# Optimization experiments

Measured on AMD Instinct MI355X. Metric: run time of the kernel, lower is better.

## Reference

```python
import jax, jax.numpy as jnp
import numpy as np
from jax import lax

B, C, D, H, W = 4, 384, 16, 16, 16
DSTATE, DCONV, EXPAND = 16, 4, 2
DIN = C * EXPAND            # 768
DTRANK = (C + 15) // 16     # 24
EPS = 1e-5


def setup_inputs() -> dict:
    ks = jax.random.split(jax.random.key(0), 12)
    g = lambda k, shape, s=0.02: jax.random.normal(k, shape, jnp.float32) * s
    return {
        "x": jax.random.normal(ks[0], (B, C, D, H, W), jnp.float32),
        "gsc_w1": g(ks[1], (C, C, 3, 3, 3)), "gsc_b1": jnp.zeros((C,), jnp.float32),
        "gsc_w2": g(ks[2], (C, C, 3, 3, 3)), "gsc_b2": jnp.zeros((C,), jnp.float32),
        "gsc_w3": g(ks[3], (C, C, 1, 1, 1)), "gsc_b3": jnp.zeros((C,), jnp.float32),
        "gsc_w4": g(ks[4], (C, C, 1, 1, 1)), "gsc_b4": jnp.zeros((C,), jnp.float32),
        "ln_g": jnp.ones((C,), jnp.float32), "ln_b": jnp.zeros((C,), jnp.float32),
        "in_proj_w": g(ks[5], (2 * DIN, C)),
        "conv1d_w": g(ks[6], (DIN, 1, DCONV), 0.1), "conv1d_b": jnp.zeros((DIN,), jnp.float32),
        "x_proj_w": g(ks[7], (DTRANK + 2 * DSTATE, DIN)),
        "dt_proj_w": g(ks[8], (DIN, DTRANK), 0.1), "dt_proj_b": jnp.full((DIN,), -4.0, jnp.float32),
        "A_log": jnp.log(jnp.tile(jnp.arange(1, DSTATE + 1, dtype=jnp.float32), (DIN, 1))),
        "D_skip": jnp.ones((DIN,), jnp.float32),
        "out_proj_w": g(ks[9], (C, DIN)),
    }


def _conv3d(x, w, b, pad):
    y = lax.conv_general_dilated(x, w, (1, 1, 1), [(pad, pad)] * 3,
                                 dimension_numbers=("NCDHW", "OIDHW", "NCDHW"))
    return y + b[None, :, None, None, None]


def _inorm(x):  # InstanceNorm3d, affine=False, biased variance
    m = x.mean((2, 3, 4), keepdims=True)
    v = x.var((2, 3, 4), keepdims=True)
    return (x - m) * lax.rsqrt(v + EPS)


def _forward(x, gsc_w1, gsc_b1, gsc_w2, gsc_b2, gsc_w3, gsc_b3, gsc_w4, gsc_b4,
             ln_g, ln_b, in_proj_w, conv1d_w, conv1d_b, x_proj_w,
             dt_proj_w, dt_proj_b, A_log, D_skip, out_proj_w):
    relu = jax.nn.relu
    # ---- GSC block (residual gated spatial conv) ----
    x1 = relu(_inorm(_conv3d(x, gsc_w1, gsc_b1, 1)))
    x1 = relu(_inorm(_conv3d(x1, gsc_w2, gsc_b2, 1)))
    x2 = relu(_inorm(_conv3d(x, gsc_w3, gsc_b3, 0)))
    xg = relu(_inorm(_conv3d(x1 + x2, gsc_w4, gsc_b4, 0))) + x
    # ---- MambaLayer: flatten voxels to tokens ----
    Bn = xg.shape[0]
    L = D * H * W
    t = xg.reshape(Bn, C, L).swapaxes(1, 2)                     # [B, L, C]
    mu = t.mean(-1, keepdims=True)
    var = t.var(-1, keepdims=True)
    tn = (t - mu) * lax.rsqrt(var + EPS) * ln_g + ln_b          # LayerNorm
    # ---- Mamba block ----
    xz = tn @ in_proj_w.T                                       # [B, L, 2*DIN]
    xin, z = jnp.split(xz, 2, axis=-1)
    xc = xin.swapaxes(1, 2)                                     # [B, DIN, L]
    xc = lax.conv_general_dilated(xc, conv1d_w, (1,), [(DCONV - 1, 0)],
                                  dimension_numbers=("NCH", "OIH", "NCH"),
                                  feature_group_count=DIN)      # causal depthwise conv
    u = jax.nn.silu(xc + conv1d_b[None, :, None]).swapaxes(1, 2)  # [B, L, DIN]
    dbl = u @ x_proj_w.T                                        # [B, L, DTRANK+2N]
    dt, Bm, Cm = jnp.split(dbl, [DTRANK, DTRANK + DSTATE], axis=-1)
    dt = jax.nn.softplus(dt @ dt_proj_w.T + dt_proj_b)          # [B, L, DIN]
    A = -jnp.exp(A_log)                                         # [DIN, N]

    def step(h, inp):  # h: [B, DIN, N]
        dt_t, B_t, C_t, u_t = inp
        dA = jnp.exp(dt_t[:, :, None] * A)
        h = dA * h + (dt_t * u_t)[:, :, None] * B_t[:, None, :]
        return h, jnp.einsum("bdn,bn->bd", h, C_t)

    h0 = jnp.zeros((Bn, DIN, DSTATE), x.dtype)
    _, ys = lax.scan(step, h0, (dt.swapaxes(0, 1), Bm.swapaxes(0, 1),
                                Cm.swapaxes(0, 1), u.swapaxes(0, 1)))
    y = ys.swapaxes(0, 1) + u * D_skip                          # [B, L, DIN]
    y = y * jax.nn.silu(z)
    out = y @ out_proj_w.T                                      # [B, L, C]
    return out.swapaxes(1, 2).reshape(Bn, C, D, H, W)


def reference(x, gsc_w1, gsc_b1, gsc_w2, gsc_b2, gsc_w3, gsc_b3, gsc_w4, gsc_b4,
              ln_g, ln_b, in_proj_w, conv1d_w, conv1d_b, x_proj_w,
              dt_proj_w, dt_proj_b, A_log, D_skip, out_proj_w):
    return _forward(x, gsc_w1, gsc_b1, gsc_w2, gsc_b2, gsc_w3, gsc_b3, gsc_w4, gsc_b4,
                    ln_g, ln_b, in_proj_w, conv1d_w, conv1d_b, x_proj_w,
                    dt_proj_w, dt_proj_b, A_log, D_skip, out_proj_w)
```

## Files before the change

### kernel.cpp

```cpp
#include <hip/hip_runtime.h>
#include <math.h>

#define CDIM 384
#define SDIM 4096
#define BDIM 4
#define DINC 768
#define NST  16
#define NCHUNK 64
#define LCHUNK 64
#define PSTRIDE 6291456

typedef unsigned short ushort_t;
typedef unsigned int uint_t;
typedef __attribute__((ext_vector_type(4))) float f32x4;
typedef __attribute__((ext_vector_type(8))) short bf16x8;

__device__ __forceinline__ ushort_t f2bf(float f) {
    union { float f; uint_t u; } v; v.f = f;
    uint_t r = v.u + 0x7FFFu + ((v.u >> 16) & 1u);
    return (ushort_t)(r >> 16);
}
__device__ __forceinline__ float bf2f(ushort_t u) {
    union { uint_t i; float f; } v; v.i = ((uint_t)u) << 16; return v.f;
}
__device__ __forceinline__ uint_t pk2(float a, float b) {
    return (uint_t)f2bf(a) | ((uint_t)f2bf(b) << 16);
}
__device__ __forceinline__ void gl16(const ushort_t* g, ushort_t* l) {
    __builtin_amdgcn_global_load_lds(
        (const __attribute__((address_space(1))) void*)(g),
        (__attribute__((address_space(3))) void*)(l), 16, 0, 0);
}

__device__ __forceinline__ void wconv_body(const float* __restrict__ W,
                                           ushort_t* __restrict__ Wb, int idx) {
    const float* wp = W + (size_t)idx * 27;
#pragma unroll
    for (int tap = 0; tap < 27; ++tap)
        Wb[(size_t)tap * (CDIM * CDIM) + idx] = f2bf(wp[tap]);
}
__device__ __forceinline__ void cvt_body(const float* __restrict__ src,
                                         ushort_t* __restrict__ dst, int i) {
    float4 v = ((const float4*)src)[i];
    uint2 o; o.x = pk2(v.x, v.y); o.y = pk2(v.z, v.w);
    ((uint2*)dst)[i] = o;
}
__global__ __launch_bounds__(256)
void prep_weights_kernel(const float* w1, const float* w2, const float* w3,
                         const float* w4, const float* ipw, const float* opw,
                         const float* xpw,
                         ushort_t* Wb1, ushort_t* Wb2, ushort_t* w3b, ushort_t* w4b,
                         ushort_t* ipwb, ushort_t* opwb, ushort_t* xpwb) {
    const int bid = blockIdx.x, t = threadIdx.x;
    if      (bid < 576)  wconv_body(w1, Wb1, bid * 256 + t);
    else if (bid < 1152) wconv_body(w2, Wb2, (bid - 576) * 256 + t);
    else if (bid < 1296) cvt_body(w3, w3b, (bid - 1152) * 256 + t);
    else if (bid < 1440) cvt_body(w4, w4b, (bid - 1296) * 256 + t);
    else if (bid < 2016) cvt_body(ipw, ipwb, (bid - 1440) * 256 + t);
    else if (bid < 2304) cvt_body(opw, opwb, (bid - 2016) * 256 + t);
    else                 cvt_body(xpw, xpwb, (bid - 2304) * 256 + t);
}

__global__ __launch_bounds__(384)
void pad_kernel(const float* __restrict__ src, ushort_t* __restrict__ Xp) {
    const int blk = blockIdx.x;
    const int b = blk >> 8, d = (blk >> 4) & 15, h = blk & 15;
    const int ci = threadIdx.x;
    const float* sp = src + (size_t)(b * CDIM + ci) * SDIM + d * 256 + h * 16;
    ushort_t* dp = Xp + ((((size_t)(b * 18 + d + 1) * 18) + (h + 1)) * 18 + 1) * CDIM + ci;
#pragma unroll
    for (int w = 0; w < 16; ++w)
        dp[(size_t)w * CDIM] = f2bf(sp[w]);
}

__global__ __launch_bounds__(384)
void pad_fuse2_kernel(const ushort_t* __restrict__ P0, const ushort_t* __restrict__ P1,
                      const float* __restrict__ stats, ushort_t* __restrict__ Xp) {
    const int blk = blockIdx.x;
    const int b = blk >> 8, d = (blk >> 4) & 15, h = blk & 15;
    const int ci = threadIdx.x;
    const size_t o = (size_t)(b * CDIM + ci) * SDIM + d * 256 + h * 16;
    const float m = stats[(b * CDIM + ci) * 2], r = stats[(b * CDIM + ci) * 2 + 1];
    union { uint4 q[2]; ushort_t u[16]; } a, c;
    a.q[0] = ((const uint4*)(P0 + o))[0]; a.q[1] = ((const uint4*)(P0 + o))[1];
    c.q[0] = ((const uint4*)(P1 + o))[0]; c.q[1] = ((const uint4*)(P1 + o))[1];
    ushort_t* dp = Xp + ((((size_t)(b * 18 + d + 1) * 18) + (h + 1)) * 18 + 1) * CDIM + ci;
#pragma unroll
    for (int w = 0; w < 16; ++w) {
        const float v = bf2f(a.u[w]) + bf2f(c.u[w]);
        dp[(size_t)w * CDIM] = f2bf(fmaxf((v - m) * r, 0.f));
    }
}

__global__ __launch_bounds__(384)
void pad_fuse3_kernel(const ushort_t* __restrict__ P0, const ushort_t* __restrict__ P1,
                      const float* __restrict__ st2, const ushort_t* __restrict__ C3,
                      const float* __restrict__ st3, ushort_t* __restrict__ Xp) {
    const int blk = blockIdx.x;
    const int b = blk >> 8, d = (blk >> 4) & 15, h = blk & 15;
    const int ci = threadIdx.x;
    const size_t o = (size_t)(b * CDIM + ci) * SDIM + d * 256 + h * 16;
    const float m2 = st2[(b * CDIM + ci) * 2], r2 = st2[(b * CDIM + ci) * 2 + 1];
    const float m3 = st3[(b * CDIM + ci) * 2], r3 = st3[(b * CDIM + ci) * 2 + 1];
    union { uint4 q[2]; ushort_t u[16]; } a, c, e;
    a.q[0] = ((const uint4*)(P0 + o))[0]; a.q[1] = ((const uint4*)(P0 + o))[1];
    c.q[0] = ((const uint4*)(P1 + o))[0]; c.q[1] = ((const uint4*)(P1 + o))[1];
    e.q[0] = ((const uint4*)(C3 + o))[0]; e.q[1] = ((const uint4*)(C3 + o))[1];
    ushort_t* dp = Xp + ((((size_t)(b * 18 + d + 1) * 18) + (h + 1)) * 18 + 1) * CDIM + ci;
#pragma unroll
    for (int w = 0; w < 16; ++w) {
        const float x1 = fmaxf((bf2f(a.u[w]) + bf2f(c.u[w]) - m2) * r2, 0.f);
        const float x2 = fmaxf((bf2f(e.u[w]) - m3) * r3, 0.f);
        dp[(size_t)w * CDIM] = f2bf(x1 + x2);
    }
}

template<int MODE>
__global__ __launch_bounds__(256)
void conv_kernel(const ushort_t* __restrict__ Xp, const ushort_t* __restrict__ Wb,
                 const ushort_t* __restrict__ W3, ushort_t* __restrict__ Y01,
                 ushort_t* __restrict__ Y2) {
    const int wid = blockIdx.x;
    const int ntid = wid & 127;
    const int rest = wid >> 7;
    const int co0 = (rest % 3) * 128;
    const int zz  = rest / 3;
    const int b  = ntid >> 5;
    const int d  = (ntid >> 1) & 15;
    const int h0 = (ntid & 1) * 8;
    const int t = threadIdx.x;
    const int lane = t & 63;
    const int wv = t >> 6;
    const int wy = wv >> 1, wx = wv & 1;

    const bool is1x1 = (MODE == 2) || (MODE == 1 && zz == 2);
    const ushort_t* Wsrc; int tap0, iters, kd0, kh0, kw0; ushort_t* Y;
    if (is1x1) {
        Wsrc = W3; tap0 = 0; iters = 12; kd0 = 1; kh0 = 1; kw0 = 1; Y = Y2;
    } else {
        Wsrc = Wb; tap0 = zz ? 14 : 0; iters = (zz ? 13 : 14) * 12;
        kd0 = zz ? 1 : 0; kh0 = zz ? 1 : 0; kw0 = zz ? 2 : 0;
        Y = Y01 + (size_t)zz * PSTRIDE;
    }

    __shared__ __align__(16) ushort_t As[2][4096];
    __shared__ __align__(16) ushort_t Bs[2][4096];

    f32x4 acc[4][4];
#pragma unroll
    for (int i = 0; i < 4; ++i)
#pragma unroll
        for (int j = 0; j < 4; ++j) acc[i][j] = (f32x4){0.f, 0.f, 0.f, 0.f};

    const int l4 = lane >> 2;
    const int cg = (((lane & 3) ^ ((lane >> 3) & 3)) << 3);
    int aTC[2], bTC[2];
#pragma unroll
    for (int i = 0; i < 2; ++i) {
        const int r = wv * 32 + i * 16 + l4;
        aTC[i] = (co0 + r) * CDIM + cg;
        bTC[i] = ((r >> 4) * 18 + (r & 15)) * CDIM + cg;
    }

    int aoff = tap0 * (CDIM * CDIM);
    int goff = (((b * 18 + d + kd0) * 18 + (h0 + kh0)) * 18 + kw0) * CDIM;
    int c12 = 0, ckw = kw0, ckh = kh0;

    const int lm = lane & 15;
    const int sw8 = (((lane >> 4) ^ ((lm >> 1) & 3)) << 3);
    const int rA0 = (wy * 64 + lm) * 32 + sw8;
    const int rB0 = (wx * 64 + lm) * 32 + sw8;

    auto stage = [&](int bf) {
        ushort_t* la = &As[bf][wv * 1024];
        ushort_t* lb = &Bs[bf][wv * 1024];
        gl16(Wsrc + aoff + aTC[0], la);
        gl16(Wsrc + aoff + aTC[1], la + 512);
        gl16(Xp + goff + bTC[0], lb);
        gl16(Xp + goff + bTC[1], lb + 512);
        aoff += 32; goff += 32;
        if (++c12 == 12) {
            c12 = 0;
            aoff += CDIM * CDIM - CDIM;
            if (++ckw == 3) {
                ckw = 0;
                if (++ckh == 3) { ckh = 0; goff += 109440; }
                else goff += 5760;
            }
        }
    };

    stage(0);
    __syncthreads();

    int buf = 0;
    for (int idx = 0; idx < iters; ++idx) {
        if (idx + 1 < iters) stage(buf ^ 1);
        bf16x8 af[4], bfr[4];
#pragma unroll
        for (int mi = 0; mi < 4; ++mi)
            af[mi] = *reinterpret_cast<const bf16x8*>(&As[buf][rA0 + mi * 512]);
#pragma unroll
        for (int ni = 0; ni < 4; ++ni)
            bfr[ni] = *reinterpret_cast<const bf16x8*>(&Bs[buf][rB0 + ni * 512]);
#pragma unroll
        for (int mi = 0; mi < 4; ++mi)
#pragma unroll
            for (int ni = 0; ni < 4; ++ni)
                acc[mi][ni] = __builtin_amdgcn_mfma_f32_16x16x32_bf16(
                    af[mi], bfr[ni], acc[mi][ni], 0, 0, 0);
        __syncthreads();
        buf ^= 1;
    }

    const int coB = co0 + wy * 64 + (lane >> 4) * 4;
    const int nB  = wx * 64 + lm;
#pragma unroll
    for (int mi = 0; mi < 4; ++mi) {
#pragma unroll
        for (int ni = 0; ni < 4; ++ni) {
            const int nl = nB + ni * 16;
            const int s = d * 256 + (h0 + (nl >> 4)) * 16 + (nl & 15);
            ushort_t* yp = Y + ((size_t)b * CDIM + (coB + mi * 16)) * SDIM + s;
#pragma unroll
            for (int j = 0; j < 4; ++j)
                yp[(size_t)j * SDIM] = f2bf(acc[mi][ni][j]);
        }
    }
}

template<int EPI>
__global__ __launch_bounds__(256)
void gemm_gl_kernel(const ushort_t* __restrict__ A, const ushort_t* __restrict__ Bw,
                    void* __restrict__ Cv, void* __restrict__ C2v,
                    int M, int N, int K, int ldc, int nx) {
    const int wid = blockIdx.x;
    const int n0 = (wid % nx) * 128;
    const int m0 = (wid / nx) * 128;
    const int t = threadIdx.x;
    const int lane = t & 63;
    const int wv = t >> 6;
    const int wy = wv >> 1, wx = wv & 1;

    __shared__ __align__(16) ushort_t As[2][4096];
    __shared__ __align__(16) ushort_t Bs[2][4096];

    f32x4 acc[4][4];
#pragma unroll
    for (int i = 0; i < 4; ++i)
#pragma unroll
        for (int j = 0; j < 4; ++j) acc[i][j] = (f32x4){0.f, 0.f, 0.f, 0.f};

    const int l4 = lane >> 2;
    const int cg = (((lane & 3) ^ ((lane >> 3) & 3)) << 3);
    size_t aTC[2], bTC[2];
#pragma unroll
    for (int i = 0; i < 2; ++i) {
        const int r = wv * 32 + i * 16 + l4;
        aTC[i] = (size_t)(m0 + r) * K + cg;
        int br = n0 + r; if (br >= N) br = N - 1;
        bTC[i] = (size_t)br * K + cg;
    }

    const int lm = lane & 15;
    const int sw8 = (((lane >> 4) ^ ((lm >> 1) & 3)) << 3);
    const int rA0 = (wy * 64 + lm) * 32 + sw8;
    const int rB0 = (wx * 64 + lm) * 32 + sw8;

    auto stage = [&](int bf, int ko) {
        ushort_t* la = &As[bf][wv * 1024];
        ushort_t* lb = &Bs[bf][wv * 1024];
        gl16(A + aTC[0] + ko, la);
        gl16(A + aTC[1] + ko, la + 512);
        gl16(Bw + bTC[0] + ko, lb);
        gl16(Bw + bTC[1] + ko, lb + 512);
    };

    const int KI = K >> 5;
    stage(0, 0);
    __syncthreads();

    int buf = 0;
    for (int kk = 0; kk < KI; ++kk) {
        if (kk + 1 < KI) stage(buf ^ 1, (kk + 1) * 32);
        bf16x8 af[4], bfr[4];
#pragma unroll
        for (int mi = 0; mi < 4; ++mi)
            af[mi] = *reinterpret_cast<const bf16x8*>(&As[buf][rA0 + mi * 512]);
#pragma unroll
        for (int ni = 0; ni < 4; ++ni)
            bfr[ni] = *reinterpret_cast<const bf16x8*>(&Bs[buf][rB0 + ni * 512]);
#pragma unroll
        for (int mi = 0; mi < 4; ++mi)
#pragma unroll
            for (int ni = 0; ni < 4; ++ni)
                acc[mi][ni] = __builtin_amdgcn_mfma_f32_16x16x32_bf16(
                    af[mi], bfr[ni], acc[mi][ni], 0, 0, 0);
        __syncthreads();
        buf ^= 1;
    }

    const int mB = m0 + wy * 64 + (lane >> 4) * 4;
    const int nB = n0 + wx * 64 + lm;
#pragma unroll
    for (int mi = 0; mi < 4; ++mi) {
#pragma unroll
        for (int ni = 0; ni < 4; ++ni) {
            const int n = nB + ni * 16;
            if (EPI == 2) {
                const int mrow = mB + mi * 16;
                const int bb = mrow >> 12, l = mrow & 4095;
                float4 st = {acc[mi][ni][0], acc[mi][ni][1],
                             acc[mi][ni][2], acc[mi][ni][3]};
                *reinterpret_cast<float4*>(
                    (float*)Cv + ((size_t)(bb * CDIM + n)) * SDIM + l) = st;
            } else {
#pragma unroll
                for (int j = 0; j < 4; ++j) {
                    const int m = mB + mi * 16 + j;
                    const float v = acc[mi][ni][j];
                    if (EPI == 0) {
                        if (n < N) ((float*)Cv)[(size_t)m * ldc + n] = v;
                    } else {
                        if (n < DINC) ((ushort_t*)Cv)[(size_t)m * DINC + n] = f2bf(v);
                        else ((ushort_t*)C2v)[(size_t)m * DINC + (n - DINC)] = f2bf(v);
                    }
                }
            }
        }
    }
}

__device__ __forceinline__ void stats_reduce(float s, float ss, float* out) {
#pragma unroll
    for (int off = 32; off > 0; off >>= 1) {
        s += __shfl_down(s, off);
        ss += __shfl_down(ss, off);
    }
    __shared__ float rs[4], rss[4];
    const int wid = threadIdx.x >> 6;
    if ((threadIdx.x & 63) == 0) { rs[wid] = s; rss[wid] = ss; }
    __syncthreads();
    if (threadIdx.x == 0) {
        float S = rs[0] + rs[1] + rs[2] + rs[3];
        float SS = rss[0] + rss[1] + rss[2] + rss[3];
        float m = S * (1.f / SDIM);
        float var = SS * (1.f / SDIM) - m * m;
        out[0] = m;
        out[1] = rsqrtf(var + 1e-5f);
    }
}

__global__ __launch_bounds__(256)
void inorm_stats_combo_kernel(const ushort_t* __restrict__ P0,
                              const ushort_t* __restrict__ P1,
                              float* __restrict__ SA,
                              const ushort_t* __restrict__ X3,
                              float* __restrict__ SB) {
    const int bid = blockIdx.x;
    float s = 0.f, ss = 0.f;
    if (bid < 1536) {
        const ushort_t* p0 = P0 + (size_t)bid * SDIM;
        const ushort_t* p1 = P1 + (size_t)bid * SDIM;
        for (int i = threadIdx.x * 8; i < SDIM; i += 2048) {
            union { uint4 q; ushort_t u[8]; } a, c;
            a.q = *(const uint4*)(p0 + i);
            c.q = *(const uint4*)(p1 + i);
#pragma unroll
            for (int j = 0; j < 8; ++j) {
                const float v = bf2f(a.u[j]) + bf2f(c.u[j]);
                s += v; ss += v * v;
            }
        }
        stats_reduce(s, ss, SA + bid * 2);
    } else {
        const int bc = bid - 1536;
        const ushort_t* xp = X3 + (size_t)bc * SDIM;
        for (int i = threadIdx.x * 8; i < SDIM; i += 2048) {
            union { uint4 q; ushort_t u[8]; } a;
            a.q = *(const uint4*)(xp + i);
#pragma unroll
            for (int j = 0; j < 8; ++j) {
                const float v = bf2f(a.u[j]);
                s += v; ss += v * v;
            }
        }
        stats_reduce(s, ss, SB + bc * 2);
    }
}

__global__ __launch_bounds__(256)
void inorm_stats_kernel(const ushort_t* __restrict__ X, float* __restrict__ stats) {
    const int bc = blockIdx.x;
    const ushort_t* xp = X + (size_t)bc * SDIM;
    float s = 0.f, ss = 0.f;
    for (int i = threadIdx.x * 8; i < SDIM; i += 2048) {
        union { uint4 q; ushort_t u[8]; } a;
        a.q = *(const uint4*)(xp + i);
#pragma unroll
        for (int j = 0; j < 8; ++j) {
            const float v = bf2f(a.u[j]);
            s += v; ss += v * v;
        }
    }
    stats_reduce(s, ss, stats + bc * 2);
}

__global__ __launch_bounds__(256)
void layernorm_kernel(const ushort_t* __restrict__ C4, const float* __restrict__ stats,
                      const float* __restrict__ X, const float* __restrict__ gam,
                      const float* __restrict__ bet, ushort_t* __restrict__ Tn) {
    const int blk = blockIdx.x;
    const int b = blk >> 7;
    const int tile0 = (blk & 127) * 32;
    const int wv = threadIdx.x >> 6;
    const int lane = threadIdx.x & 63;
    const int l0 = tile0 + wv * 8;

    __shared__ ushort_t tile[32 * 384];

    float v[6][8];
    float s[8], ss[8];
#pragma unroll
    for (int t = 0; t < 8; ++t) { s[t] = 0.f; ss[t] = 0.f; }
    float g[6], be[6];

#pragma unroll
    for (int i = 0; i < 6; ++i) {
        const int c = lane + i * 64;
        g[i] = gam[c]; be[i] = bet[c];
        const size_t base = (size_t)(b * CDIM + c) * SDIM + l0;
        union { uint4 q; ushort_t u[8]; } cv;
        cv.q = *(const uint4*)(C4 + base);
        const float4 x0 = *(const float4*)(X + base);
        const float4 x1 = *(const float4*)(X + base + 4);
        const float xs[8] = {x0.x, x0.y, x0.z, x0.w, x1.x, x1.y, x1.z, x1.w};
        const float m = stats[(b * CDIM + c) * 2];
        const float r = stats[(b * CDIM + c) * 2 + 1];
#pragma unroll
        for (int t = 0; t < 8; ++t) {
            const float val = fmaxf((bf2f(cv.u[t]) - m) * r, 0.f) + xs[t];
            v[i][t] = val;
            s[t] += val; ss[t] += val * val;
        }
    }
#pragma unroll
    for (int off = 32; off > 0; off >>= 1) {
#pragma unroll
        for (int t = 0; t < 8; ++t) {
            s[t] += __shfl_xor(s[t], off);
            ss[t] += __shfl_xor(ss[t], off);
        }
    }
#pragma unroll
    for (int t = 0; t < 8; ++t) {
        const float mean = s[t] * (1.f / CDIM);
        const float rstd = rsqrtf(ss[t] * (1.f / CDIM) - mean * mean + 1e-5f);
        const int trow = (wv * 8 + t) * 384;
#pragma unroll
        for (int i = 0; i < 6; ++i) {
            const int c = lane + i * 64;
            tile[trow + c] = f2bf((v[i][t] - mean) * rstd * g[i] + be[i]);
        }
    }
    __syncthreads();
    uint4* dst = (uint4*)(Tn + ((size_t)b * 4096 + tile0) * CDIM);
    const uint4* srcp = (const uint4*)tile;
#pragma unroll
    for (int k = 0; k < 6; ++k)
        dst[k * 256 + threadIdx.x] = srcp[k * 256 + threadIdx.x];
}

__global__ __launch_bounds__(256)
void gemm_dtproj_kernel(const float* __restrict__ A, const float* __restrict__ B,
                        ushort_t* __restrict__ C, const float* __restrict__ bias,
                        int M, int N, int K, int lda, int ldb, int ldc) {
    __shared__ __align__(16) float As[16][132];
    __shared__ __align__(16) float Bs[16][68];
    const int t = threadIdx.x;
    const int m0 = blockIdx.y * 128;
    const int n0 = blockIdx.x * 64;

    float acc[8][4];
#pragma unroll
    for (int i = 0; i < 8; ++i)
#pragma unroll
        for (int j = 0; j < 4; ++j) acc[i][j] = 0.f;

    const int mr = (t & 15) * 8;
    const int nr = (t >> 4) * 4;

    for (int k0 = 0; k0 < K; k0 += 16) {
#pragma unroll
        for (int idx = 0; idx < 8; ++idx) {
            const int e = idx * 256 + t;
            const int k = e & 15, m = e >> 4;
            float v = 0.f;
            if (k0 + k < K) v = A[(size_t)(m0 + m) * lda + (k0 + k)];
            As[k][m] = v;
        }
#pragma unroll
        for (int idx = 0; idx < 4; ++idx) {
            const int e = idx * 256 + t;
            const int k = e & 15, n = e >> 4;
            float v = 0.f;
            if ((n0 + n) < N && (k0 + k) < K) v = B[(size_t)(n0 + n) * ldb + (k0 + k)];
            Bs[k][n] = v;
        }
        __syncthreads();
#pragma unroll
        for (int k = 0; k < 16; ++k) {
            float4 a0 = *(const float4*)&As[k][mr];
            float4 a1 = *(const float4*)&As[k][mr + 4];
            float4 b0 = *(const float4*)&Bs[k][nr];
            const float av[8] = {a0.x, a0.y, a0.z, a0.w, a1.x, a1.y, a1.z, a1.w};
            const float bv[4] = {b0.x, b0.y, b0.z, b0.w};
#pragma unroll
            for (int i = 0; i < 8; ++i)
#pragma unroll
                for (int j = 0; j < 4; ++j)
                    acc[i][j] = fmaf(av[i], bv[j], acc[i][j]);
        }
        __syncthreads();
    }

#pragma unroll
    for (int i = 0; i < 8; ++i) {
        const int m = m0 + mr + i;
#pragma unroll
        for (int j = 0; j < 4; ++j) {
            const int n = n0 + nr + j;
            if (n >= N) continue;
            float v = acc[i][j] + bias[n];
            v = (v > 20.f) ? v : log1pf(__expf(v));
            C[(size_t)m * ldc + n] = f2bf(v);
        }
    }
}

__global__ __launch_bounds__(256)
void dwconv_silu_kernel(const ushort_t* __restrict__ Xin, const float* __restrict__ W,
                        const float* __restrict__ bias, ushort_t* __restrict__ U) {
    const int dch = blockIdx.x * 256 + threadIdx.x;
    const int l0 = blockIdx.y * 4, b = blockIdx.z;
    const float4 w4 = ((const float4*)W)[dch];
    const float wk[4] = {w4.x, w4.y, w4.z, w4.w};
    const float bs = bias[dch];
    const size_t base = ((size_t)b * 4096 + l0) * DINC + dch;
    float r[7];
#pragma unroll
    for (int k = 0; k < 7; ++k) {
        const int ll = l0 - 3 + k;
        r[k] = (ll >= 0) ? bf2f(Xin[base + (size_t)(k - 3) * DINC]) : 0.f;
    }
#pragma unroll
    for (int j = 0; j < 4; ++j) {
        float acc = bs;
#pragma unroll
        for (int k = 0; k < 4; ++k) acc = fmaf(r[j + k], wk[k], acc);
        U[base + (size_t)j * DINC] = f2bf(acc / (1.f + __expf(-acc)));
    }
}

__global__ __launch_bounds__(256)
void scan_phase1_kernel(const ushort_t* __restrict__ DT, const ushort_t* __restrict__ U,
                        const float* __restrict__ DBL, const float* __restrict__ A_log,
                        float* __restrict__ HOUT, float* __restrict__ SDT) {
    const int b = blockIdx.z, chunk = blockIdx.y;
    const int dch = blockIdx.x * 256 + threadIdx.x;
    float Arow[16];
#pragma unroll
    for (int n = 0; n < NST; ++n) Arow[n] = -__expf(A_log[dch * NST + n]);

    __shared__ float bcs[LCHUNK][16];
    const size_t tokbase = (size_t)b * 4096 + chunk * LCHUNK;
#pragma unroll
    for (int idx = 0; idx < 4; ++idx) {
        const int e = idx * 256 + threadIdx.x;
        bcs[e >> 4][e & 15] = DBL[(tokbase + (e >> 4)) * 56 + 24 + (e & 15)];
    }
    __syncthreads();

    size_t off = tokbase * DINC + dch;
    float h[16];
#pragma unroll
    for (int n = 0; n < NST; ++n) h[n] = 0.f;
    float sdt = 0.f;
    float cdt = bf2f(DT[off]), cu = bf2f(U[off]);
    for (int t = 0; t < LCHUNK; ++t) {
        float ndt = 0.f, nu = 0.f;
        if (t < LCHUNK - 1) { ndt = bf2f(DT[off + DINC]); nu = bf2f(U[off + DINC]); }
        sdt += cdt;
        const float du = cdt * cu;
#pragma unroll
        for (int n = 0; n < NST; ++n)
            h[n] = __expf(cdt * Arow[n]) * h[n] + du * bcs[t][n];
        off += DINC;
        cdt = ndt; cu = nu;
    }
    float* hp = HOUT + (((size_t)(b * DINC + dch) * NCHUNK + chunk) << 4);
#pragma unroll
    for (int n = 0; n < NST; ++n) hp[n] = h[n];
    SDT[(size_t)(b * DINC + dch) * NCHUNK + chunk] = sdt;
}

__global__ __launch_bounds__(256)
void scan_phase2_kernel(float* __restrict__ HOUT, const float* __restrict__ SDT,
                        const float* __restrict__ A_log) {
    const int t = blockIdx.x * 256 + threadIdx.x;
    const int b = t / (DINC * NST);
    const int rem = t - b * (DINC * NST);
    const int d = rem >> 4, n = rem & 15;
    const float An = -__expf(A_log[d * NST + n]);
    float* hp = HOUT + (((size_t)(b * DINC + d) * NCHUNK) << 4) + n;
    const float* sp = SDT + (size_t)(b * DINC + d) * NCHUNK;
    float H = 0.f;
    for (int c = 0; c < NCHUNK; ++c) {
        const float tmp = hp[c * 16];
        const float dA = __expf(An * sp[c]);
        hp[c * 16] = H;
        H = dA * H + tmp;
    }
}

__global__ __launch_bounds__(256)
void scan_phase3_kernel(ushort_t* __restrict__ DT, const ushort_t* __restrict__ U,
                        const float* __restrict__ DBL, const ushort_t* __restrict__ Z,
                        const float* __restrict__ A_log, const float* __restrict__ D_skip,
                        const float* __restrict__ HOUT) {
    const int b = blockIdx.z, chunk = blockIdx.y;
    const int dch = blockIdx.x * 256 + threadIdx.x;
    float Arow[16];
#pragma unroll
    for (int n = 0; n < NST; ++n) Arow[n] = -__expf(A_log[dch * NST + n]);
    const float Dsk = D_skip[dch];

    __shared__ float bcs[LCHUNK][32];
    const size_t tokbase = (size_t)b * 4096 + chunk * LCHUNK;
#pragma unroll
    for (int idx = 0; idx < 8; ++idx) {
        const int e = idx * 256 + threadIdx.x;
        bcs[e >> 5][e & 31] = DBL[(tokbase + (e >> 5)) * 56 + 24 + (e & 31)];
    }
    __syncthreads();

    float h[16];
    const float* hp = HOUT + (((size_t)(b * DINC + dch) * NCHUNK + chunk) << 4);
#pragma unroll
    for (int n = 0; n < NST; ++n) h[n] = hp[n];

    size_t off = tokbase * DINC + dch;
    float cdt = bf2f(DT[off]), cu = bf2f(U[off]), cz = bf2f(Z[off]);
    for (int t = 0; t < LCHUNK; ++t) {
        float ndt = 0.f, nu = 0.f, nz = 0.f;
        if (t < LCHUNK - 1) {
            ndt = bf2f(DT[off + DINC]); nu = bf2f(U[off + DINC]); nz = bf2f(Z[off + DINC]);
        }
        const float du = cdt * cu;
        float y = 0.f;
#pragma unroll
        for (int n = 0; n < NST; ++n) {
            h[n] = __expf(cdt * Arow[n]) * h[n] + du * bcs[t][n];
            y = fmaf(h[n], bcs[t][16 + n], y);
        }
        y += cu * Dsk;
        const float sz = cz / (1.f + __expf(-cz));
        DT[off] = f2bf(y * sz);
        off += DINC;
        cdt = ndt; cu = nu; cz = nz;
    }
}

extern "C" void kernel_launch(void* const* d_in, const int* in_sizes, int n_in,
                              void* d_out, int out_size, void* d_ws, size_t ws_size,
                              hipStream_t stream) {
    (void)in_sizes; (void)n_in; (void)out_size; (void)ws_size;
    const float* x         = (const float*)d_in[0];
    const float* w1        = (const float*)d_in[1];
    const float* w2        = (const float*)d_in[3];
    const float* w3        = (const float*)d_in[5];
    const float* w4        = (const float*)d_in[7];
    const float* ln_g      = (const float*)d_in[9];
    const float* ln_b      = (const float*)d_in[10];
    const float* in_proj_w = (const float*)d_in[11];
    const float* conv1d_w  = (const float*)d_in[12];
    const float* conv1d_b  = (const float*)d_in[13];
    const float* x_proj_w  = (const float*)d_in[14];
    const float* dt_proj_w = (const float*)d_in[15];
    const float* dt_proj_b = (const float*)d_in[16];
    const float* A_log     = (const float*)d_in[17];
    const float* D_skip    = (const float*)d_in[18];
    const float* out_proj_w= (const float*)d_in[19];
    float* out = (float*)d_out;

    float* ws = (float*)d_ws;
    float* R0 = ws;
    float* R1 = ws + 6291456;
    float* R2 = ws + 12582912;
    float* R3 = ws + 25165824;
    float* R4 = ws + 37748736;

    ushort_t* P0    = (ushort_t*)R0;
    ushort_t* P1    = P0 + PSTRIDE;
    ushort_t* C34   = (ushort_t*)R3;
    ushort_t* Wb1   = (ushort_t*)R2;
    ushort_t* Xp    = (ushort_t*)(R2 + 2097152);
    ushort_t* w3b   = (ushort_t*)(R2 + 6576128);
    ushort_t* w4b   = (ushort_t*)(R2 + 6649856);
    ushort_t* Wb2   = (ushort_t*)(R2 + 6723584);
    float*    SA    = R4;
    float*    SB    = R4 + 4096;
    ushort_t* ipwb  = (ushort_t*)(R4 + 6291456);
    ushort_t* opwb  = (ushort_t*)(R4 + 6586368);
    ushort_t* xpwb  = (ushort_t*)(R4 + 6733824);
    ushort_t* tnb   = (ushort_t*)R0;
    float*    DBL   = R0 + 3145728;
    float*    HOUT  = R1;
    float*    SDT   = R1 + 3145728;
    ushort_t* XIN   = (ushort_t*)R2;
    ushort_t* Zb    = (ushort_t*)R3;
    ushort_t* Ub    = (ushort_t*)R4;
    ushort_t* DTb   = (ushort_t*)R2;

    const size_t XP_BYTES = (size_t)4 * 18 * 18 * 18 * CDIM * 2;

    hipMemsetAsync(Xp, 0, XP_BYTES, stream);
    prep_weights_kernel<<<2346, 256, 0, stream>>>(
        w1, w2, w3, w4, in_proj_w, out_proj_w, x_proj_w,
        Wb1, Wb2, w3b, w4b, ipwb, opwb, xpwb);
    pad_kernel<<<1024, 384, 0, stream>>>(x, Xp);
    conv_kernel<1><<<1152, 256, 0, stream>>>(Xp, Wb1, w3b, P0, C34);
    inorm_stats_combo_kernel<<<3072, 256, 0, stream>>>(P0, P1, SA, C34, SB);
    pad_fuse2_kernel<<<1024, 384, 0, stream>>>(P0, P1, SA, Xp);
    conv_kernel<0><<<768, 256, 0, stream>>>(Xp, Wb2, nullptr, P0, nullptr);
    inorm_stats_combo_kernel<<<1536, 256, 0, stream>>>(P0, P1, SA, nullptr, nullptr);
    pad_fuse3_kernel<<<1024, 384, 0, stream>>>(P0, P1, SA, C34, SB, Xp);
    conv_kernel<2><<<384, 256, 0, stream>>>(Xp, nullptr, w4b, nullptr, C34);
    inorm_stats_kernel<<<1536, 256, 0, stream>>>(C34, SA);
    layernorm_kernel<<<512, 256, 0, stream>>>(C34, SA, x, ln_g, ln_b, tnb);
    gemm_gl_kernel<1><<<1536, 256, 0, stream>>>(
        tnb, ipwb, XIN, Zb, 16384, 1536, CDIM, 0, 12);
    dwconv_silu_kernel<<<dim3(3, 1024, 4), 256, 0, stream>>>(XIN, conv1d_w, conv1d_b, Ub);
    gemm_gl_kernel<0><<<128, 256, 0, stream>>>(
        Ub, xpwb, DBL, nullptr, 16384, 56, DINC, 56, 1);
    gemm_dtproj_kernel<<<dim3(12, 128), 256, 0, stream>>>(
        DBL, dt_proj_w, DTb, dt_proj_b, 16384, DINC, 24, 56, 24, DINC);
    scan_phase1_kernel<<<dim3(3, NCHUNK, 4), 256, 0, stream>>>(
        DTb, Ub, DBL, A_log, HOUT, SDT);
    scan_phase2_kernel<<<192, 256, 0, stream>>>(HOUT, SDT, A_log);
    scan_phase3_kernel<<<dim3(3, NCHUNK, 4), 256, 0, stream>>>(
        DTb, Ub, DBL, Zb, A_log, D_skip, HOUT);
    gemm_gl_kernel<2><<<384, 256, 0, stream>>>(
        DTb, opwb, out, nullptr, 16384, CDIM, DINC, 0, 3);
}
```

Before: 746.3 us.

## Enlarge conv implicit-GEMM tile to 128x256 with 8 waves, single-buffered LDS

The conv kernel now uses 512-thread blocks (8 waves in a 2x4 layout), each computing 128 output channels by 256 spatial positions, a full 16x16 plane. Each block reuses its weight tile across twice as many voxels, which halves weight traffic, and the grid halves. The LDS double buffer is replaced by a single buffer with load, sync, compute, sync, so global loads no longer overlap MFMA work inside a block. The bet is that the larger reuse and more resident waves hide latency better than explicit prefetching did, at the risk of exposed load latency and fewer blocks (384 for the 3x3x3 conv).

```diff
diff --git a/kernel.cpp b/kernel.cpp
--- a/kernel.cpp
+++ b/kernel.cpp
@@ -116,22 +116,21 @@
 }
 
 template<int MODE>
-__global__ __launch_bounds__(256)
+__global__ __launch_bounds__(512)
 void conv_kernel(const ushort_t* __restrict__ Xp, const ushort_t* __restrict__ Wb,
                  const ushort_t* __restrict__ W3, ushort_t* __restrict__ Y01,
                  ushort_t* __restrict__ Y2) {
     const int wid = blockIdx.x;
-    const int ntid = wid & 127;
-    const int rest = wid >> 7;
+    const int ntid = wid & 63;
+    const int rest = wid >> 6;
     const int co0 = (rest % 3) * 128;
     const int zz  = rest / 3;
-    const int b  = ntid >> 5;
-    const int d  = (ntid >> 1) & 15;
-    const int h0 = (ntid & 1) * 8;
+    const int b  = ntid >> 4;
+    const int d  = ntid & 15;
     const int t = threadIdx.x;
     const int lane = t & 63;
     const int wv = t >> 6;
-    const int wy = wv >> 1, wx = wv & 1;
+    const int wy = wv >> 2, wx = wv & 3;
 
     const bool is1x1 = (MODE == 2) || (MODE == 1 && zz == 2);
     const ushort_t* Wsrc; int tap0, iters, kd0, kh0, kw0; ushort_t* Y;
@@ -143,8 +142,8 @@
         Y = Y01 + (size_t)zz * PSTRIDE;
     }
 
-    __shared__ __align__(16) ushort_t As[2][4096];
-    __shared__ __align__(16) ushort_t Bs[2][4096];
+    __shared__ __align__(16) ushort_t As[4096];
+    __shared__ __align__(16) ushort_t Bs[8192];
 
     f32x4 acc[4][4];
 #pragma unroll
@@ -154,16 +153,19 @@
 
     const int l4 = lane >> 2;
     const int cg = (((lane & 3) ^ ((lane >> 3) & 3)) << 3);
-    int aTC[2], bTC[2];
+    const int rA = wv * 16 + l4;
+    const int aTC = (co0 + rA) * CDIM + cg;
+    int bTC[2];
 #pragma unroll
     for (int i = 0; i < 2; ++i) {
         const int r = wv * 32 + i * 16 + l4;
-        aTC[i] = (co0 + r) * CDIM + cg;
         bTC[i] = ((r >> 4) * 18 + (r & 15)) * CDIM + cg;
     }
+    ushort_t* lA = &As[wv * 512];
+    ushort_t* lB[2] = { &Bs[wv * 1024], &Bs[wv * 1024 + 512] };
 
     int aoff = tap0 * (CDIM * CDIM);
-    int goff = (((b * 18 + d + kd0) * 18 + (h0 + kh0)) * 18 + kw0) * CDIM;
+    int goff = (((b * 18 + d + kd0) * 18 + kh0) * 18 + kw0) * CDIM;
     int c12 = 0, ckw = kw0, ckh = kh0;
 
     const int lm = lane & 15;
@@ -171,13 +173,10 @@
     const int rA0 = (wy * 64 + lm) * 32 + sw8;
     const int rB0 = (wx * 64 + lm) * 32 + sw8;
 
-    auto stage = [&](int bf) {
-        ushort_t* la = &As[bf][wv * 1024];
-        ushort_t* lb = &Bs[bf][wv * 1024];
-        gl16(Wsrc + aoff + aTC[0], la);
-        gl16(Wsrc + aoff + aTC[1], la + 512);
-        gl16(Xp + goff + bTC[0], lb);
-        gl16(Xp + goff + bTC[1], lb + 512);
+    for (int idx = 0; idx < iters; ++idx) {
+        gl16(Wsrc + aoff + aTC, lA);
+        gl16(Xp + goff + bTC[0], lB[0]);
+        gl16(Xp + goff + bTC[1], lB[1]);
         aoff += 32; goff += 32;
         if (++c12 == 12) {
             c12 = 0;
@@ -188,21 +187,14 @@
                 else goff += 5760;
             }
         }
-    };
-
-    stage(0);
-    __syncthreads();
-
-    int buf = 0;
-    for (int idx = 0; idx < iters; ++idx) {
-        if (idx + 1 < iters) stage(buf ^ 1);
+        __syncthreads();
         bf16x8 af[4], bfr[4];
 #pragma unroll
         for (int mi = 0; mi < 4; ++mi)
-            af[mi] = *reinterpret_cast<const bf16x8*>(&As[buf][rA0 + mi * 512]);
+            af[mi] = *reinterpret_cast<const bf16x8*>(&As[rA0 + mi * 512]);
 #pragma unroll
         for (int ni = 0; ni < 4; ++ni)
-            bfr[ni] = *reinterpret_cast<const bf16x8*>(&Bs[buf][rB0 + ni * 512]);
+            bfr[ni] = *reinterpret_cast<const bf16x8*>(&Bs[rB0 + ni * 512]);
 #pragma unroll
         for (int mi = 0; mi < 4; ++mi)
 #pragma unroll
@@ -210,17 +202,15 @@
                 acc[mi][ni] = __builtin_amdgcn_mfma_f32_16x16x32_bf16(
                     af[mi], bfr[ni], acc[mi][ni], 0, 0, 0);
         __syncthreads();
-        buf ^= 1;
     }
 
     const int coB = co0 + wy * 64 + (lane >> 4) * 4;
-    const int nB  = wx * 64 + lm;
 #pragma unroll
     for (int mi = 0; mi < 4; ++mi) {
 #pragma unroll
         for (int ni = 0; ni < 4; ++ni) {
-            const int nl = nB + ni * 16;
-            const int s = d * 256 + (h0 + (nl >> 4)) * 16 + (nl & 15);
+            const int nl = wx * 64 + ni * 16 + lm;
+            const int s = d * 256 + nl;
             ushort_t* yp = Y + ((size_t)b * CDIM + (coB + mi * 16)) * SDIM + s;
 #pragma unroll
             for (int j = 0; j < 4; ++j)
@@ -729,13 +719,13 @@
         w1, w2, w3, w4, in_proj_w, out_proj_w, x_proj_w,
         Wb1, Wb2, w3b, w4b, ipwb, opwb, xpwb);
     pad_kernel<<<1024, 384, 0, stream>>>(x, Xp);
-    conv_kernel<1><<<1152, 256, 0, stream>>>(Xp, Wb1, w3b, P0, C34);
+    conv_kernel<1><<<576, 512, 0, stream>>>(Xp, Wb1, w3b, P0, C34);
     inorm_stats_combo_kernel<<<3072, 256, 0, stream>>>(P0, P1, SA, C34, SB);
     pad_fuse2_kernel<<<1024, 384, 0, stream>>>(P0, P1, SA, Xp);
-    conv_kernel<0><<<768, 256, 0, stream>>>(Xp, Wb2, nullptr, P0, nullptr);
+    conv_kernel<0><<<384, 512, 0, stream>>>(Xp, Wb2, nullptr, P0, nullptr);
     inorm_stats_combo_kernel<<<1536, 256, 0, stream>>>(P0, P1, SA, nullptr, nullptr);
     pad_fuse3_kernel<<<1024, 384, 0, stream>>>(P0, P1, SA, C34, SB, Xp);
-    conv_kernel<2><<<384, 256, 0, stream>>>(Xp, nullptr, w4b, nullptr, C34);
+    conv_kernel<2><<<192, 512, 0, stream>>>(Xp, nullptr, w4b, nullptr, C34);
     inorm_stats_kernel<<<1536, 256, 0, stream>>>(C34, SA);
     layernorm_kernel<<<512, 256, 0, stream>>>(C34, SA, x, ln_g, ln_b, tnb);
     gemm_gl_kernel<1><<<1536, 256, 0, stream>>>(
```

After: 731.3 us, median of 2. 2.0% less time.
